# Performance work log

Measured on AMD Instinct MI355X. Metric: run time of the kernel, lower is better.

Reference implementation:

```python
import jax, jax.numpy as jnp
import numpy as np

EPS = 1e-12
B, L_IN, D = 8, 4096, 256
T_OUT = 1024


def setup_inputs() -> dict:
    key = jax.random.key(0)
    kx, kl = jax.random.split(key)
    x = jax.random.normal(kx, (B, L_IN, D), dtype=jnp.float32)
    # ragged prefix lengths in [L_IN//2, L_IN]
    lengths = jax.random.randint(kl, (B,), L_IN // 2, L_IN + 1)
    mask = jnp.arange(L_IN)[None, :] < lengths[:, None]  # [B, L_in] bool, False = pad
    return {"x": x, "mask": mask, "finallength": T_OUT}


def reference(x, mask, finallength):
    """Faithful batched version of Change_length.forward(x, finallength, mask, getstd=True).

    padded_out: area interpolation == adaptive average pooling (integer bins,
                uniform weights: [floor(j*L/T), ceil((j+1)*L/T)) ).
    std_out:    fractional-overlap weight matrix W, mean/var via W @ seq.
    """
    Bb, L, Dd = x.shape
    T = int(finallength)
    dtype = x.dtype

    # compact valid tokens to the front (handles arbitrary masks; stable order)
    idx = jnp.argsort(jnp.logical_not(mask), axis=1, stable=True)  # [B, L]
    seq = jnp.take_along_axis(x, idx[:, :, None], axis=1)          # [B, L, D]
    Lb = jnp.sum(mask, axis=1)                                     # [B] int
    valid = (jnp.arange(L)[None, :] < Lb[:, None])                 # [B, L]
    seq = seq * valid[:, :, None].astype(dtype)

    Lf = Lb.astype(dtype)[:, None, None]                           # [B,1,1]
    j = jnp.arange(T, dtype=dtype)[None, :, None]                  # [1,T,1]
    i = jnp.arange(L, dtype=dtype)[None, None, :]                  # [1,1,L]

    # ---- adaptive avg pool (F.interpolate mode='area') for the mean output ----
    s_idx = jnp.floor(j * Lf / T)                                  # [B,T,1]
    e_idx = jnp.ceil((j + 1.0) * Lf / T)                           # [B,T,1]
    A = ((i >= s_idx) & (i < e_idx)).astype(dtype)                 # [B,T,L]
    A = A / jnp.maximum(e_idx - s_idx, 1.0)
    padded_out = jnp.einsum('btl,bld->btd', A, seq)                # [B,T,D]

    # ---- fractional-overlap weight matrix for std ----
    step = Lf / T                                                  # [B,1,1]
    start = j * step
    end = start + step
    W = jnp.clip(jnp.minimum(i + 1.0, end) - jnp.maximum(i, start), 0.0)  # [B,T,L]
    Wsum = jnp.clip(jnp.sum(W, axis=2, keepdims=True), EPS)        # [B,T,1]
    mean = jnp.einsum('btl,bld->btd', W, seq) / Wsum
    mean_sq = jnp.einsum('btl,bld->btd', W, seq * seq) / Wsum
    var = jnp.clip(mean_sq - mean * mean, EPS)
    std_out = jnp.sqrt(var)                                        # [B,T,D]

    out_mask = jnp.ones((Bb, T), dtype=bool)                       # fixed T, all valid
    return padded_out, out_mask, std_out
```

## Files before the change

kernel.cpp:

```cpp
#include <hip/hip_runtime.h>
#include <hip/hip_bf16.h>
#include <math.h>

#define BB   8
#define LL   4096
#define DD   256
#define TT   1024
#define EPSV 1e-12f

__global__ __launch_bounds__(256) void changelen_fused(const float* __restrict__ x,
                                                       const void* __restrict__ mask,
                                                       float* __restrict__ out) {
    const int wave = threadIdx.x >> 6;
    const int lane = threadIdx.x & 63;
    const int bt   = (blockIdx.x << 2) + wave;
    const int b    = bt >> 10;
    const int t    = bt & (TT - 1);

    const int* mi32 = (const int*)mask;
    const unsigned char* mu8 = (const unsigned char*)mask;
    const bool is_i32 = (mi32[0] == 1);

    bool p1;
    if (is_i32) p1 = (mi32[(size_t)b * LL + lane * 64 + 63] != 0);
    else        p1 = (mu8 [(size_t)b * LL + lane * 64 + 63] != 0);
    const int n1 = __popcll(__ballot(p1));
    int Lbi;
    if (n1 == 64) {
        Lbi = LL;
    } else {
        const int base = n1 << 6;
        bool p2;
        if (is_i32) p2 = (mi32[(size_t)b * LL + base + lane] != 0);
        else        p2 = (mu8 [(size_t)b * LL + base + lane] != 0);
        Lbi = base + __popcll(__ballot(p2));
    }

    const float Lb    = (float)Lbi;
    const float step  = Lb * (1.0f / (float)TT);
    const float start = (float)t * step;
    const float end   = start + step;
    const float s_f   = floorf(start);
    const float e_f   = ceilf(end);
    const int   s     = (int)s_f;
    const int   e     = (int)e_f;
    const float inv_cnt = 1.0f / fmaxf(e_f - s_f, 1.0f);

    float4 v[5];
    const float* xb = x + (size_t)b * LL * DD;
    #pragma unroll
    for (int k = 0; k < 5; ++k) {
        int row = s + k;
        row = row < (LL - 1) ? row : (LL - 1);
        v[k] = ((const float4*)(xb + (size_t)row * DD))[lane];
    }

    float4 sumA = {0.f, 0.f, 0.f, 0.f};
    float4 sw   = {0.f, 0.f, 0.f, 0.f};
    float4 sw2  = {0.f, 0.f, 0.f, 0.f};
    #pragma unroll
    for (int k = 0; k < 5; ++k) {
        const float fi = (float)(s + k);
        float w = fminf(fi + 1.0f, end) - fmaxf(fi, start);
        w = fmaxf(w, 0.0f);
        const float am = (s + k < e) ? inv_cnt : 0.0f;
        sumA.x = fmaf(am, v[k].x, sumA.x); sumA.y = fmaf(am, v[k].y, sumA.y);
        sumA.z = fmaf(am, v[k].z, sumA.z); sumA.w = fmaf(am, v[k].w, sumA.w);
        sw.x = fmaf(w, v[k].x, sw.x); sw.y = fmaf(w, v[k].y, sw.y);
        sw.z = fmaf(w, v[k].z, sw.z); sw.w = fmaf(w, v[k].w, sw.w);
        sw2.x = fmaf(w, v[k].x * v[k].x, sw2.x); sw2.y = fmaf(w, v[k].y * v[k].y, sw2.y);
        sw2.z = fmaf(w, v[k].z * v[k].z, sw2.z); sw2.w = fmaf(w, v[k].w * v[k].w, sw2.w);
    }

    float4 stdv;
    {
        const float inv_s = 1.0f / step;
        const float mx = sw.x * inv_s, my = sw.y * inv_s, mz = sw.z * inv_s, mw = sw.w * inv_s;
        const float qx = sw2.x * inv_s, qy = sw2.y * inv_s, qz = sw2.z * inv_s, qw = sw2.w * inv_s;
        stdv.x = sqrtf(fmaxf(qx - mx * mx, EPSV));
        stdv.y = sqrtf(fmaxf(qy - my * my, EPSV));
        stdv.z = sqrtf(fmaxf(qz - mz * mz, EPSV));
        stdv.w = sqrtf(fmaxf(qw - mw * mw, EPSV));
    }

    float4* out4 = (float4*)out;
    const size_t o_pool4 = (size_t)bt * (DD / 4) + (size_t)lane;
    const size_t std_base4 = ((size_t)BB * TT * DD + (size_t)BB * TT) / 4;
    out4[o_pool4] = sumA;
    out4[std_base4 + o_pool4] = stdv;
    if (lane == 0) {
        out[(size_t)BB * TT * DD + (size_t)bt] = 1.0f;
    }
}

extern "C" void kernel_launch(void* const* d_in, const int* in_sizes, int n_in,
                              void* d_out, int out_size, void* d_ws, size_t ws_size,
                              hipStream_t stream) {
    const float* x    = (const float*)d_in[0];
    const void*  mask = d_in[1];
    float* out = (float*)d_out;

    changelen_fused<<<(BB * TT) / 4, 256, 0, stream>>>(x, mask, out);
}
```

Baseline: 82.60 us.

## Split mask length scan into prep kernel and skip unneeded row loads

Moves the per-batch valid-length computation and the out_mask fill into a single-block prep kernel that writes lengths to workspace. The main kernel then reads one int per block instead of redoing ballot scans of the mask in every wave. It also loads rows 3 and 4 only when the bin spans them. This adds a second launch and a serial dependency on a one-block kernel in exchange for less redundant mask traffic and fewer global loads.

Result: no change. 83.10 us (+0.6%).

```diff
diff --git a/kernel.cpp b/kernel.cpp
--- a/kernel.cpp
+++ b/kernel.cpp
@@ -1,5 +1,4 @@
 #include <hip/hip_runtime.h>
-#include <hip/hip_bf16.h>
 #include <math.h>
 
 #define BB   8
@@ -8,33 +7,50 @@
 #define TT   1024
 #define EPSV 1e-12f
 
-__global__ __launch_bounds__(256) void changelen_fused(const float* __restrict__ x,
-                                                       const void* __restrict__ mask,
-                                                       float* __restrict__ out) {
+__global__ __launch_bounds__(256) void changelen_prep(const void* __restrict__ mask,
+                                                      int* __restrict__ lb,
+                                                      float* __restrict__ out) {
     const int wave = threadIdx.x >> 6;
     const int lane = threadIdx.x & 63;
-    const int bt   = (blockIdx.x << 2) + wave;
-    const int b    = bt >> 10;
-    const int t    = bt & (TT - 1);
-
     const int* mi32 = (const int*)mask;
     const unsigned char* mu8 = (const unsigned char*)mask;
     const bool is_i32 = (mi32[0] == 1);
 
-    bool p1;
-    if (is_i32) p1 = (mi32[(size_t)b * LL + lane * 64 + 63] != 0);
-    else        p1 = (mu8 [(size_t)b * LL + lane * 64 + 63] != 0);
-    const int n1 = __popcll(__ballot(p1));
-    int Lbi;
-    if (n1 == 64) {
-        Lbi = LL;
-    } else {
-        const int base = n1 << 6;
-        bool p2;
-        if (is_i32) p2 = (mi32[(size_t)b * LL + base + lane] != 0);
-        else        p2 = (mu8 [(size_t)b * LL + base + lane] != 0);
-        Lbi = base + __popcll(__ballot(p2));
+    for (int b = wave; b < BB; b += 4) {
+        bool p1;
+        if (is_i32) p1 = (mi32[(size_t)b * LL + lane * 64 + 63] != 0);
+        else        p1 = (mu8 [(size_t)b * LL + lane * 64 + 63] != 0);
+        const int n1 = __popcll(__ballot(p1));
+        int Lbi;
+        if (n1 == 64) {
+            Lbi = LL;
+        } else {
+            const int base = n1 << 6;
+            bool p2;
+            if (is_i32) p2 = (mi32[(size_t)b * LL + base + lane] != 0);
+            else        p2 = (mu8 [(size_t)b * LL + base + lane] != 0);
+            Lbi = base + __popcll(__ballot(p2));
+        }
+        if (lane == 0) lb[b] = Lbi;
     }
+
+    const float4 ones = {1.f, 1.f, 1.f, 1.f};
+    float4* m4 = (float4*)(out + (size_t)BB * TT * DD);
+    #pragma unroll
+    for (int i = 0; i < (BB * TT) / (4 * 256); ++i)
+        m4[i * 256 + threadIdx.x] = ones;
+}
+
+__global__ __launch_bounds__(256) void changelen_main(const float* __restrict__ x,
+                                                      const int* __restrict__ lb,
+                                                      float* __restrict__ out) {
+    const int wave = threadIdx.x >> 6;
+    const int lane = threadIdx.x & 63;
+    const int bt   = (blockIdx.x << 2) + wave;
+    const int b    = blockIdx.x >> 8;
+    const int t    = bt & (TT - 1);
+
+    const int Lbi = lb[b];
 
     const float Lb    = (float)Lbi;
     const float step  = Lb * (1.0f / (float)TT);
@@ -43,34 +59,47 @@
     const float s_f   = floorf(start);
     const float e_f   = ceilf(end);
     const int   s     = (int)s_f;
-    const int   e     = (int)e_f;
+    const int   cnt   = (int)e_f - s;
     const float inv_cnt = 1.0f / fmaxf(e_f - s_f, 1.0f);
 
-    float4 v[5];
     const float* xb = x + (size_t)b * LL * DD;
-    #pragma unroll
-    for (int k = 0; k < 5; ++k) {
-        int row = s + k;
-        row = row < (LL - 1) ? row : (LL - 1);
-        v[k] = ((const float4*)(xb + (size_t)row * DD))[lane];
-    }
+    const float4* r0 = (const float4*)(xb + (size_t)s * DD);
+
+    float4 v0 = r0[lane];
+    float4 v1 = r0[64 + lane];
+    const int o2 = (s + 2 < LL) ? 128 : 64;
+    float4 v2 = r0[o2 + lane];
+    float4 v3 = {0.f, 0.f, 0.f, 0.f};
+    float4 v4 = {0.f, 0.f, 0.f, 0.f};
+    if (cnt > 3) v3 = r0[192 + lane];
+    if (cnt > 4) v4 = r0[256 + lane];
 
     float4 sumA = {0.f, 0.f, 0.f, 0.f};
     float4 sw   = {0.f, 0.f, 0.f, 0.f};
     float4 sw2  = {0.f, 0.f, 0.f, 0.f};
-    #pragma unroll
-    for (int k = 0; k < 5; ++k) {
-        const float fi = (float)(s + k);
-        float w = fminf(fi + 1.0f, end) - fmaxf(fi, start);
-        w = fmaxf(w, 0.0f);
-        const float am = (s + k < e) ? inv_cnt : 0.0f;
-        sumA.x = fmaf(am, v[k].x, sumA.x); sumA.y = fmaf(am, v[k].y, sumA.y);
-        sumA.z = fmaf(am, v[k].z, sumA.z); sumA.w = fmaf(am, v[k].w, sumA.w);
-        sw.x = fmaf(w, v[k].x, sw.x); sw.y = fmaf(w, v[k].y, sw.y);
-        sw.z = fmaf(w, v[k].z, sw.z); sw.w = fmaf(w, v[k].w, sw.w);
-        sw2.x = fmaf(w, v[k].x * v[k].x, sw2.x); sw2.y = fmaf(w, v[k].y * v[k].y, sw2.y);
-        sw2.z = fmaf(w, v[k].z * v[k].z, sw2.z); sw2.w = fmaf(w, v[k].w * v[k].w, sw2.w);
+
+#define ACC(K, V)                                                              \
+    {                                                                          \
+        const float fi = (float)(s + (K));                                     \
+        float w = fminf(fi + 1.0f, end) - fmaxf(fi, start);                    \
+        w = fmaxf(w, 0.0f);                               \
+        const float am = ((K) < cnt) ? inv_cnt : 0.0f;                         \
+        sumA.x = fmaf(am, (V).x, sumA.x); sumA.y = fmaf(am, (V).y, sumA.y);    \
+        sumA.z = fmaf(am, (V).z, sumA.z); sumA.w = fmaf(am, (V).w, sumA.w);    \
+        sw.x = fmaf(w, (V).x, sw.x); sw.y = fmaf(w, (V).y, sw.y);              \
+        sw.z = fmaf(w, (V).z, sw.z); sw.w = fmaf(w, (V).w, sw.w);              \
+        sw2.x = fmaf(w, (V).x * (V).x, sw2.x);                                 \
+        sw2.y = fmaf(w, (V).y * (V).y, sw2.y);                                 \
+        sw2.z = fmaf(w, (V).z * (V).z, sw2.z);                                 \
+        sw2.w = fmaf(w, (V).w * (V).w, sw2.w);                                 \
     }
+
+    ACC(0, v0)
+    ACC(1, v1)
+    ACC(2, v2)
+    ACC(3, v3)
+    ACC(4, v4)
+#undef ACC
 
     float4 stdv;
     {
@@ -84,13 +113,10 @@
     }
 
     float4* out4 = (float4*)out;
-    const size_t o_pool4 = (size_t)bt * (DD / 4) + (size_t)lane;
+    const size_t o4 = (size_t)bt * (DD / 4) + (size_t)lane;
     const size_t std_base4 = ((size_t)BB * TT * DD + (size_t)BB * TT) / 4;
-    out4[o_pool4] = sumA;
-    out4[std_base4 + o_pool4] = stdv;
-    if (lane == 0) {
-        out[(size_t)BB * TT * DD + (size_t)bt] = 1.0f;
-    }
+    out4[o4] = sumA;
+    out4[std_base4 + o4] = stdv;
 }
 
 extern "C" void kernel_launch(void* const* d_in, const int* in_sizes, int n_in,
@@ -99,6 +125,8 @@
     const float* x    = (const float*)d_in[0];
     const void*  mask = d_in[1];
     float* out = (float*)d_out;
+    int*   lb  = (int*)d_ws;
 
-    changelen_fused<<<(BB * TT) / 4, 256, 0, stream>>>(x, mask, out);
+    changelen_prep<<<1, 256, 0, stream>>>(mask, lb, out);
+    changelen_main<<<(BB * TT) / 4, 256, 0, stream>>>(x, lb, out);
 }
```
